# Optimization experiments

Hardware: AMD Instinct MI355X
Metric: run time of the kernel (lower is better)

Reference implementation:

```python
import jax, jax.numpy as jnp
import numpy as np

H, C = 3, 64  # heads, per-head channels
NEG_SLOPE = 0.2

def setup_inputs() -> dict:
    key = jax.random.key(0)
    ks = jax.random.split(key, 8)
    B, N, D, E = 2, 50000, 128, 800000
    h = jax.random.normal(ks[0], (B, N, D), dtype=jnp.float32)
    edge_index = jax.random.randint(ks[1], (2, E), 0, N, dtype=jnp.int64)
    s = 1.0 / np.sqrt(D)
    W = jax.random.normal(ks[2], (D, H * C), dtype=jnp.float32) * s
    a_src = jax.random.normal(ks[3], (H, C), dtype=jnp.float32) * (1.0 / np.sqrt(C))
    a_dst = jax.random.normal(ks[4], (H, C), dtype=jnp.float32) * (1.0 / np.sqrt(C))
    bias = jnp.zeros((H * C,), dtype=jnp.float32)
    Wo = jax.random.normal(ks[5], (H * C, 1), dtype=jnp.float32) * (1.0 / np.sqrt(H * C))
    bo = jnp.zeros((1,), dtype=jnp.float32)
    return {"h": h, "edge_index": edge_index, "W": W, "a_src": a_src,
            "a_dst": a_dst, "bias": bias, "Wo": Wo, "bo": bo}

def _gat_single(h_b, src, dst, N, W, a_src, a_dst, bias):
    # h_b: [N, D] -> x: [N, H, C]
    x = (h_b @ W).reshape(-1, H, C)
    alpha_s = jnp.einsum('nhc,hc->nh', x, a_src)  # [N, H]
    alpha_d = jnp.einsum('nhc,hc->nh', x, a_dst)  # [N, H]
    e = alpha_s[src] + alpha_d[dst]               # [E', H]
    e = jnp.where(e > 0, e, NEG_SLOPE * e)        # leaky_relu(0.2)
    # segment softmax over edges grouped by destination node
    emax = jax.ops.segment_max(e, dst, num_segments=N)          # [N, H]
    p = jnp.exp(e - emax[dst])
    denom = jax.ops.segment_sum(p, dst, num_segments=N)         # [N, H]
    att = p / (denom[dst] + 1e-16)                               # [E', H]
    out = jax.ops.segment_sum(att[:, :, None] * x[src], dst, num_segments=N)  # [N,H,C]
    return out.reshape(-1, H * C) + bias

def reference(h, edge_index, W, a_src, a_dst, bias, Wo, bo):
    B, N, D = h.shape
    # PyG GATConv default: add self loops
    loops = jnp.arange(N, dtype=edge_index.dtype)
    src = jnp.concatenate([edge_index[0], loops])
    dst = jnp.concatenate([edge_index[1], loops])
    gat = jax.vmap(lambda hb: _gat_single(hb, src, dst, N, W, a_src, a_dst, bias))(h)
    gat = jax.nn.elu(gat)            # [B, N, H*C]; dropout inactive (eval)
    logits = gat @ Wo + bo           # [B, N, 1]
    return logits
```

## Files before the change

### kernel.cpp

```cpp
#include <hip/hip_runtime.h>
#include <hip/hip_bf16.h>
#include <math.h>

typedef __hip_bfloat16 bf16;
typedef __attribute__((ext_vector_type(8))) short short8;
typedef __attribute__((ext_vector_type(4))) short short4v;
typedef __attribute__((ext_vector_type(4))) float f32x4;

#define HC 192
#define DIN 128
#define NEG_SLOPE 0.2f
#define GN 4
#define CAP 56
#define GROWS 128

static inline int cdiv(int a, int b){ return (a + b - 1) / b; }

__device__ inline short f2bf(float f){
  __hip_bfloat16 b = __float2bfloat16(f);
  return __builtin_bit_cast(short, b);
}
__device__ inline float loadf(const void* p, size_t i, int fm){
  return fm ? __bfloat162float(((const bf16*)p)[i]) : ((const float*)p)[i];
}
__device__ inline int eload(const void* p, long long i, int em){
  return em ? (int)(((const long long*)p)[i]) : ((const int*)p)[i];
}
__device__ inline unsigned pack2h(float a, float b){
  unsigned short ha = __builtin_bit_cast(unsigned short, (_Float16)a);
  unsigned short hb = __builtin_bit_cast(unsigned short, (_Float16)b);
  return (unsigned)ha | ((unsigned)hb << 16);
}
__device__ inline float unph(unsigned w, int hi){
  unsigned short hs = hi ? (unsigned short)(w >> 16) : (unsigned short)(w & 0xffff);
  return (float)__builtin_bit_cast(_Float16, hs);
}

__device__ inline int detect_fm(const unsigned* __restrict__ hw){
  unsigned w = hw[threadIdx.x & 63];
  unsigned expo = (w >> 7) & 0xFF;
  unsigned long long m = __ballot(expo >= 100 && expo <= 135);
  return __popcll(m) > 32;
}
__device__ inline int detect_em(const unsigned* __restrict__ ew){
  unsigned long long m = __ballot(ew[2*(threadIdx.x & 63) + 1] != 0);
  return __popcll(m) < 32;
}

__global__ void k_repack(const void* __restrict__ W, const void* __restrict__ a_src,
    const void* __restrict__ a_dst, const void* __restrict__ bias,
    const void* __restrict__ Wo, const void* __restrict__ bo,
    const unsigned* __restrict__ hw, bf16* __restrict__ Wt,
    float* __restrict__ asf, float* __restrict__ adf, float* __restrict__ biasf,
    float* __restrict__ Wof, float* __restrict__ bof,
    int* __restrict__ counts, int N){
  int fm = detect_fm(hw);
  int idx = blockIdx.x * 256 + threadIdx.x;
  for (int i = idx; i < N; i += 96 * 256) counts[i] = 0;
  if (idx < DIN * HC){
    int d = idx / HC, j = idx - d * HC;
    Wt[j * DIN + d] = __float2bfloat16(loadf(W, idx, fm));
  }
  if (idx < HC){
    asf[idx]   = loadf(a_src, idx, fm);
    adf[idx]   = loadf(a_dst, idx, fm);
    biasf[idx] = loadf(bias, idx, fm);
    Wof[idx]   = loadf(Wo, idx, fm);
  }
  if (idx == 0) bof[0] = loadf(bo, 0, fm);
}

__global__ __launch_bounds__(512) void k_gemm(const void* __restrict__ h,
    const bf16* __restrict__ Wt, bf16* __restrict__ x,
    const float* __restrict__ asf, const float* __restrict__ adf,
    float* __restrict__ asp, float* __restrict__ adp, int M, int N){
  int fm   = detect_fm((const unsigned*)h);
  int tid  = threadIdx.x;
  int w    = tid >> 6;
  int lane = tid & 63;
  int r16  = lane & 15;
  int quad = lane >> 4;
  __shared__ short ldsW[HC * 136];
  for (int c = tid; c < HC * 16; c += 512){
    int row = c >> 4, kg = c & 15;
    *(short8*)&ldsW[row * 136 + kg * 8] = *(const short8*)(Wt + row * DIN + kg * 8);
  }
  __syncthreads();

  int row  = blockIdx.x * GROWS + w * 16 + r16;
  int lrow = min(row, M - 1);
  f32x4 acc[12];
  #pragma unroll
  for (int i = 0; i < 12; i++) acc[i] = (f32x4){0.f,0.f,0.f,0.f};
  size_t hbase = (size_t)lrow * DIN + quad * 8;
  #pragma unroll
  for (int kb = 0; kb < 4; kb++){
    short8 bh;
    if (fm == 0){
      const float* hf = (const float*)h + hbase + kb * 32;
      float4 a = *(const float4*)hf;
      float4 b = *(const float4*)(hf + 4);
      bh[0]=f2bf(a.x); bh[1]=f2bf(a.y); bh[2]=f2bf(a.z); bh[3]=f2bf(a.w);
      bh[4]=f2bf(b.x); bh[5]=f2bf(b.y); bh[6]=f2bf(b.z); bh[7]=f2bf(b.w);
    } else {
      bh = *(const short8*)((const bf16*)h + hbase + kb * 32);
    }
    #pragma unroll
    for (int nt = 0; nt < 12; nt++){
      short8 aw = *(const short8*)&ldsW[(nt*16 + r16) * 136 + kb * 32 + quad * 8];
      acc[nt] = __builtin_amdgcn_mfma_f32_16x16x32_bf16(aw, bh, acc[nt], 0,0,0);
    }
  }
  if (row < M){
    #pragma unroll
    for (int nt = 0; nt < 12; nt++){
      short4v pk = { f2bf(acc[nt][0]), f2bf(acc[nt][1]),
                     f2bf(acc[nt][2]), f2bf(acc[nt][3]) };
      *(short4v*)(x + (size_t)row * HC + nt*16 + quad*4) = pk;
    }
  }
  float vs[3] = {0.f,0.f,0.f}, vd[3] = {0.f,0.f,0.f};
  #pragma unroll
  for (int nt = 0; nt < 12; nt++){
    int hh = nt >> 2;
    f32x4 a4 = *(const f32x4*)(asf + nt*16 + quad*4);
    f32x4 d4 = *(const f32x4*)(adf + nt*16 + quad*4);
    vs[hh] += acc[nt][0]*a4[0] + acc[nt][1]*a4[1] + acc[nt][2]*a4[2] + acc[nt][3]*a4[3];
    vd[hh] += acc[nt][0]*d4[0] + acc[nt][1]*d4[1] + acc[nt][2]*d4[2] + acc[nt][3]*d4[3];
  }
  #pragma unroll
  for (int hh = 0; hh < 3; hh++){
    float v1 = vs[hh], v2 = vd[hh];
    v1 += __shfl_down(v1, 32);  v1 += __shfl_down(v1, 16);
    v2 += __shfl_down(v2, 32);  v2 += __shfl_down(v2, 16);
    if (lane < 16 && row < M){
      int b = row >= N;
      int node = row - b * N;
      asp[(size_t)node*8 + b*3 + hh] = v1;
      adp[(size_t)node*8 + b*3 + hh] = v2;
    }
  }
}

__global__ void k_scatter(const void* __restrict__ ei, int E, int N,
    int* __restrict__ counts, const float* __restrict__ asp,
    const float* __restrict__ adp, uint4* __restrict__ pe){
  int em = detect_em((const unsigned*)ei);
  int idx = blockIdx.x * 256 + threadIdx.x;
  if (idx >= E + N) return;
  int s, d;
  if (idx < E){
    s = eload(ei, idx, em);
    d = eload(ei, (long long)E + idx, em);
  } else { s = d = idx - E; }
  if ((unsigned)d >= (unsigned)N) return;
  if ((unsigned)s >= (unsigned)N) s = 0;
  int slot = atomicAdd(&counts[d], 1);
  if (slot >= CAP) return;
  float4 A0 = ((const float4*)asp)[(size_t)s*2];
  float4 A1 = ((const float4*)asp)[(size_t)s*2 + 1];
  float4 D0 = ((const float4*)adp)[(size_t)d*2];
  float4 D1 = ((const float4*)adp)[(size_t)d*2 + 1];
  float e0 = A0.x + D0.x, e1 = A0.y + D0.y, e2 = A0.z + D0.z;
  float e3 = A0.w + D0.w, e4 = A1.x + D1.x, e5 = A1.y + D1.y;
  e0 = e0 > 0.f ? e0 : NEG_SLOPE*e0;  e1 = e1 > 0.f ? e1 : NEG_SLOPE*e1;
  e2 = e2 > 0.f ? e2 : NEG_SLOPE*e2;  e3 = e3 > 0.f ? e3 : NEG_SLOPE*e3;
  e4 = e4 > 0.f ? e4 : NEG_SLOPE*e4;  e5 = e5 > 0.f ? e5 : NEG_SLOPE*e5;
  uint4 rec;
  rec.x = pack2h(__expf(e0), __expf(e1));
  rec.y = pack2h(__expf(e2), __expf(e3));
  rec.z = pack2h(__expf(e4), __expf(e5));
  rec.w = (unsigned)s;
  pe[(size_t)d*CAP + slot] = rec;
}

__global__ __launch_bounds__(192) void k_gat(const bf16* __restrict__ x,
    const uint4* __restrict__ pe, const int* __restrict__ cnt,
    const float* __restrict__ biasf, const float* __restrict__ Wof,
    const float* __restrict__ bof, float* __restrict__ out, int N){
  int blk  = blockIdx.x;
  int t    = threadIdx.x;
  int node = t / 48;
  int u    = t - node * 48;
  int b    = u >= 24;
  int c8   = u - b * 24;
  int hh   = c8 >> 3;
  __shared__ int   cs[GN];
  __shared__ uint4 ldsR[GN * CAP];
  __shared__ float red[192];
  if (t < GN) cs[t] = min(cnt[GN*blk + t], CAP);
  __syncthreads();
  for (int j = t; j < GN * CAP; j += 192){
    int nd = j / CAP, sl = j - nd * CAP;
    if (sl < cs[nd]) ldsR[j] = pe[(size_t)(GN*blk + nd) * CAP + sl];
  }
  __syncthreads();
  int mycnt = cs[node];
  const ushort* xb = (const ushort*)x + (size_t)b * N * HC + c8 * 8;
  int pidx = b*3 + hh;
  int pw_i = pidx >> 1, pw_h = pidx & 1;
  const unsigned* ldsU = (const unsigned*)ldsR;
  float acc[8];
  #pragma unroll
  for (int k = 0; k < 8; k++) acc[k] = 0.f;
  float den = 0.f;
  int rbase = node * CAP;
  #pragma unroll 8
  for (int i = 0; i < mycnt; i++){
    int rec = rbase + i;
    float p = unph(ldsU[rec*4 + pw_i], pw_h);
    int s   = (int)ldsU[rec*4 + 3];
    uint4 q = *(const uint4*)(xb + (size_t)s * HC);
    den += p;
    acc[0] = fmaf(p, __uint_as_float(q.x << 16),         acc[0]);
    acc[1] = fmaf(p, __uint_as_float(q.x & 0xffff0000u), acc[1]);
    acc[2] = fmaf(p, __uint_as_float(q.y << 16),         acc[2]);
    acc[3] = fmaf(p, __uint_as_float(q.y & 0xffff0000u), acc[3]);
    acc[4] = fmaf(p, __uint_as_float(q.z << 16),         acc[4]);
    acc[5] = fmaf(p, __uint_as_float(q.z & 0xffff0000u), acc[5]);
    acc[6] = fmaf(p, __uint_as_float(q.w << 16),         acc[6]);
    acc[7] = fmaf(p, __uint_as_float(q.w & 0xffff0000u), acc[7]);
  }
  float inv = 1.f / (den + 1e-16f);
  float4 bi0 = ((const float4*)biasf)[c8*2], bi1 = ((const float4*)biasf)[c8*2+1];
  float4 w0  = ((const float4*)Wof)[c8*2],  w1  = ((const float4*)Wof)[c8*2+1];
  float r = 0.f;
  {
    float v;
    v = acc[0]*inv + bi0.x; v = v > 0.f ? v : expm1f(v); r += v * w0.x;
    v = acc[1]*inv + bi0.y; v = v > 0.f ? v : expm1f(v); r += v * w0.y;
    v = acc[2]*inv + bi0.z; v = v > 0.f ? v : expm1f(v); r += v * w0.z;
    v = acc[3]*inv + bi0.w; v = v > 0.f ? v : expm1f(v); r += v * w0.w;
    v = acc[4]*inv + bi1.x; v = v > 0.f ? v : expm1f(v); r += v * w1.x;
    v = acc[5]*inv + bi1.y; v = v > 0.f ? v : expm1f(v); r += v * w1.y;
    v = acc[6]*inv + bi1.z; v = v > 0.f ? v : expm1f(v); r += v * w1.z;
    v = acc[7]*inv + bi1.w; v = v > 0.f ? v : expm1f(v); r += v * w1.w;
  }
  red[t] = r;
  __syncthreads();
  if (t < 64){
    int g = t >> 3, l = t & 7;
    float v = red[g*24 + l] + red[g*24 + 8 + l] + red[g*24 + 16 + l];
    v += __shfl_down(v, 4, 8);
    v += __shfl_down(v, 2, 8);
    v += __shfl_down(v, 1, 8);
    if (l == 0){
      int nd = GN*blk + (g >> 1);
      int bb = g & 1;
      out[(size_t)bb * N + nd] = v + bof[0];
    }
  }
}

extern "C" void kernel_launch(void* const* d_in, const int* in_sizes, int n_in,
                              void* d_out, int out_size, void* d_ws, size_t ws_size,
                              hipStream_t stream){
  const void* h     = d_in[0];
  const void* ei    = d_in[1];
  const void* W     = d_in[2];
  const void* a_src = d_in[3];
  const void* a_dst = d_in[4];
  const void* bias  = d_in[5];
  const void* Wo    = d_in[6];
  const void* bo    = d_in[7];
  float* out = (float*)d_out;

  const int M    = in_sizes[0] / DIN;
  const int N    = M / 2;
  const int E    = in_sizes[1] / 2;
  const int Etot = E + N;

  char* ws = (char*)d_ws;
  size_t off = 0;
  auto alloc = [&](size_t bytes) -> void* {
    void* p = ws + off;
    off = (off + bytes + 511) & ~(size_t)511;
    return p;
  };
  bf16*  x       = (bf16*) alloc((size_t)M * HC * sizeof(bf16));
  float* asp     = (float*)alloc((size_t)N * 8 * sizeof(float));
  float* adp     = (float*)alloc((size_t)N * 8 * sizeof(float));
  int*   counts  = (int*)  alloc((size_t)N * sizeof(int));
  uint4* pe      = (uint4*)alloc((size_t)N * CAP * sizeof(uint4));
  bf16*  Wt      = (bf16*) alloc((size_t)DIN * HC * sizeof(bf16));
  float* asf     = (float*)alloc(HC * sizeof(float));
  float* adf     = (float*)alloc(HC * sizeof(float));
  float* biasf   = (float*)alloc(HC * sizeof(float));
  float* Wof     = (float*)alloc(HC * sizeof(float));
  float* bof     = (float*)alloc(16 * sizeof(float));
  (void)ws_size; (void)n_in; (void)out_size;

  k_repack<<<96, 256, 0, stream>>>(W, a_src, a_dst, bias, Wo, bo,
      (const unsigned*)h, Wt, asf, adf, biasf, Wof, bof, counts, N);
  k_gemm<<<cdiv(M, GROWS), 512, 0, stream>>>(h, Wt, x, asf, adf, asp, adp, M, N);
  k_scatter<<<cdiv(Etot, 256), 256, 0, stream>>>(ei, E, N, counts, asp, adp, pe);
  k_gat<<<N / GN, 192, 0, stream>>>(x, pe, counts, biasf, Wof, bof, out, N);
}
```

Before: 264.2 us.

## Bucket edge sources only and recompute attention logits inside aggregation kernel

```diff
diff --git a/kernel.cpp b/kernel.cpp
--- a/kernel.cpp
+++ b/kernel.cpp
@@ -25,15 +25,6 @@
 }
 __device__ inline int eload(const void* p, long long i, int em){
   return em ? (int)(((const long long*)p)[i]) : ((const int*)p)[i];
-}
-__device__ inline unsigned pack2h(float a, float b){
-  unsigned short ha = __builtin_bit_cast(unsigned short, (_Float16)a);
-  unsigned short hb = __builtin_bit_cast(unsigned short, (_Float16)b);
-  return (unsigned)ha | ((unsigned)hb << 16);
-}
-__device__ inline float unph(unsigned w, int hi){
-  unsigned short hs = hi ? (unsigned short)(w >> 16) : (unsigned short)(w & 0xffff);
-  return (float)__builtin_bit_cast(_Float16, hs);
 }
 
 __device__ inline int detect_fm(const unsigned* __restrict__ hw){
@@ -68,6 +59,23 @@
     Wof[idx]   = loadf(Wo, idx, fm);
   }
   if (idx == 0) bof[0] = loadf(bo, 0, fm);
+}
+
+__global__ void k_bucket(const void* __restrict__ ei, int E, int N,
+    int* __restrict__ counts, unsigned* __restrict__ srcs){
+  int em = detect_em((const unsigned*)ei);
+  int idx = blockIdx.x * 256 + threadIdx.x;
+  if (idx >= E + N) return;
+  int s, d;
+  if (idx < E){
+    s = eload(ei, idx, em);
+    d = eload(ei, (long long)E + idx, em);
+  } else { s = d = idx - E; }
+  if ((unsigned)d >= (unsigned)N) return;
+  if ((unsigned)s >= (unsigned)N) s = 0;
+  int slot = atomicAdd(&counts[d], 1);
+  if (slot >= CAP) return;
+  srcs[(size_t)d * CAP + slot] = (unsigned)s;
 }
 
 __global__ __launch_bounds__(512) void k_gemm(const void* __restrict__ h,
@@ -112,11 +120,14 @@
     }
   }
   if (row < M){
+    int bb    = row >= N;
+    int nodeR = row - bb * N;
+    bf16* xr  = x + ((size_t)nodeR * 2 + bb) * HC;
     #pragma unroll
     for (int nt = 0; nt < 12; nt++){
       short4v pk = { f2bf(acc[nt][0]), f2bf(acc[nt][1]),
                      f2bf(acc[nt][2]), f2bf(acc[nt][3]) };
-      *(short4v*)(x + (size_t)row * HC + nt*16 + quad*4) = pk;
+      *(short4v*)(xr + nt*16 + quad*4) = pk;
     }
   }
   float vs[3] = {0.f,0.f,0.f}, vd[3] = {0.f,0.f,0.f};
@@ -142,40 +153,9 @@
   }
 }
 
-__global__ void k_scatter(const void* __restrict__ ei, int E, int N,
-    int* __restrict__ counts, const float* __restrict__ asp,
-    const float* __restrict__ adp, uint4* __restrict__ pe){
-  int em = detect_em((const unsigned*)ei);
-  int idx = blockIdx.x * 256 + threadIdx.x;
-  if (idx >= E + N) return;
-  int s, d;
-  if (idx < E){
-    s = eload(ei, idx, em);
-    d = eload(ei, (long long)E + idx, em);
-  } else { s = d = idx - E; }
-  if ((unsigned)d >= (unsigned)N) return;
-  if ((unsigned)s >= (unsigned)N) s = 0;
-  int slot = atomicAdd(&counts[d], 1);
-  if (slot >= CAP) return;
-  float4 A0 = ((const float4*)asp)[(size_t)s*2];
-  float4 A1 = ((const float4*)asp)[(size_t)s*2 + 1];
-  float4 D0 = ((const float4*)adp)[(size_t)d*2];
-  float4 D1 = ((const float4*)adp)[(size_t)d*2 + 1];
-  float e0 = A0.x + D0.x, e1 = A0.y + D0.y, e2 = A0.z + D0.z;
-  float e3 = A0.w + D0.w, e4 = A1.x + D1.x, e5 = A1.y + D1.y;
-  e0 = e0 > 0.f ? e0 : NEG_SLOPE*e0;  e1 = e1 > 0.f ? e1 : NEG_SLOPE*e1;
-  e2 = e2 > 0.f ? e2 : NEG_SLOPE*e2;  e3 = e3 > 0.f ? e3 : NEG_SLOPE*e3;
-  e4 = e4 > 0.f ? e4 : NEG_SLOPE*e4;  e5 = e5 > 0.f ? e5 : NEG_SLOPE*e5;
-  uint4 rec;
-  rec.x = pack2h(__expf(e0), __expf(e1));
-  rec.y = pack2h(__expf(e2), __expf(e3));
-  rec.z = pack2h(__expf(e4), __expf(e5));
-  rec.w = (unsigned)s;
-  pe[(size_t)d*CAP + slot] = rec;
-}
-
 __global__ __launch_bounds__(192) void k_gat(const bf16* __restrict__ x,
-    const uint4* __restrict__ pe, const int* __restrict__ cnt,
+    const unsigned* __restrict__ srcs, const int* __restrict__ cnt,
+    const float* __restrict__ asp, const float* __restrict__ adp,
     const float* __restrict__ biasf, const float* __restrict__ Wof,
     const float* __restrict__ bof, float* __restrict__ out, int N){
   int blk  = blockIdx.x;
@@ -185,21 +165,21 @@
   int b    = u >= 24;
   int c8   = u - b * 24;
   int hh   = c8 >> 3;
-  __shared__ int   cs[GN];
-  __shared__ uint4 ldsR[GN * CAP];
-  __shared__ float red[192];
+  __shared__ int      cs[GN];
+  __shared__ unsigned ldsS[GN * CAP];
+  __shared__ float    red[192];
   if (t < GN) cs[t] = min(cnt[GN*blk + t], CAP);
   __syncthreads();
   for (int j = t; j < GN * CAP; j += 192){
     int nd = j / CAP, sl = j - nd * CAP;
-    if (sl < cs[nd]) ldsR[j] = pe[(size_t)(GN*blk + nd) * CAP + sl];
+    if (sl < cs[nd]) ldsS[j] = srcs[(size_t)(GN*blk + nd) * CAP + sl];
   }
   __syncthreads();
   int mycnt = cs[node];
-  const ushort* xb = (const ushort*)x + (size_t)b * N * HC + c8 * 8;
-  int pidx = b*3 + hh;
-  int pw_i = pidx >> 1, pw_h = pidx & 1;
-  const unsigned* ldsU = (const unsigned*)ldsR;
+  int d     = GN*blk + node;
+  int pidx  = b*3 + hh;
+  float adv = adp[(size_t)d * 8 + pidx];
+  const ushort* xb = (const ushort*)x + (size_t)b * HC + c8 * 8;
   float acc[8];
   #pragma unroll
   for (int k = 0; k < 8; k++) acc[k] = 0.f;
@@ -207,10 +187,11 @@
   int rbase = node * CAP;
   #pragma unroll 8
   for (int i = 0; i < mycnt; i++){
-    int rec = rbase + i;
-    float p = unph(ldsU[rec*4 + pw_i], pw_h);
-    int s   = (int)ldsU[rec*4 + 3];
-    uint4 q = *(const uint4*)(xb + (size_t)s * HC);
+    int s   = (int)ldsS[rbase + i];
+    float e = asp[(size_t)s * 8 + pidx] + adv;
+    e = e > 0.f ? e : NEG_SLOPE * e;
+    float p = __expf(e);
+    uint4 q = *(const uint4*)(xb + (size_t)s * (2 * HC));
     den += p;
     acc[0] = fmaf(p, __uint_as_float(q.x << 16),         acc[0]);
     acc[1] = fmaf(p, __uint_as_float(q.x & 0xffff0000u), acc[1]);
@@ -277,22 +258,22 @@
     off = (off + bytes + 511) & ~(size_t)511;
     return p;
   };
-  bf16*  x       = (bf16*) alloc((size_t)M * HC * sizeof(bf16));
-  float* asp     = (float*)alloc((size_t)N * 8 * sizeof(float));
-  float* adp     = (float*)alloc((size_t)N * 8 * sizeof(float));
-  int*   counts  = (int*)  alloc((size_t)N * sizeof(int));
-  uint4* pe      = (uint4*)alloc((size_t)N * CAP * sizeof(uint4));
-  bf16*  Wt      = (bf16*) alloc((size_t)DIN * HC * sizeof(bf16));
-  float* asf     = (float*)alloc(HC * sizeof(float));
-  float* adf     = (float*)alloc(HC * sizeof(float));
-  float* biasf   = (float*)alloc(HC * sizeof(float));
-  float* Wof     = (float*)alloc(HC * sizeof(float));
-  float* bof     = (float*)alloc(16 * sizeof(float));
+  bf16*     x      = (bf16*)    alloc((size_t)M * HC * sizeof(bf16));
+  float*    asp    = (float*)   alloc((size_t)N * 8 * sizeof(float));
+  float*    adp    = (float*)   alloc((size_t)N * 8 * sizeof(float));
+  int*      counts = (int*)     alloc((size_t)N * sizeof(int));
+  unsigned* srcs   = (unsigned*)alloc((size_t)N * CAP * sizeof(unsigned));
+  bf16*     Wt     = (bf16*)    alloc((size_t)DIN * HC * sizeof(bf16));
+  float*    asf    = (float*)   alloc(HC * sizeof(float));
+  float*    adf    = (float*)   alloc(HC * sizeof(float));
+  float*    biasf  = (float*)   alloc(HC * sizeof(float));
+  float*    Wof    = (float*)   alloc(HC * sizeof(float));
+  float*    bof    = (float*)   alloc(16 * sizeof(float));
   (void)ws_size; (void)n_in; (void)out_size;
 
   k_repack<<<96, 256, 0, stream>>>(W, a_src, a_dst, bias, Wo, bo,
       (const unsigned*)h, Wt, asf, adf, biasf, Wof, bof, counts, N);
+  k_bucket<<<cdiv(Etot, 256), 256, 0, stream>>>(ei, E, N, counts, srcs);
   k_gemm<<<cdiv(M, GROWS), 512, 0, stream>>>(h, Wt, x, asf, adf, asp, adp, M, N);
-  k_scatter<<<cdiv(Etot, 256), 256, 0, stream>>>(ei, E, N, counts, asp, adp, pe);
-  k_gat<<<N / GN, 192, 0, stream>>>(x, pe, counts, biasf, Wof, bof, out, N);
-}
+  k_gat<<<N / GN, 192, 0, stream>>>(x, srcs, counts, asp, adp, biasf, Wof, bof, out, N);
+}
```

After: 280.9 us. +6.3%, slower.

## Precompute attention logits via folded W·a, overlap edge bucketing with GEMM

Applied to the files above, without the earlier changes.

```diff
diff --git a/kernel.cpp b/kernel.cpp
--- a/kernel.cpp
+++ b/kernel.cpp
@@ -47,47 +47,152 @@
   return __popcll(m) < 32;
 }
 
-__global__ void k_repack(const void* __restrict__ W, const void* __restrict__ a_src,
+__global__ void k_zero(const void* __restrict__ W, const void* __restrict__ a_src,
     const void* __restrict__ a_dst, const void* __restrict__ bias,
     const void* __restrict__ Wo, const void* __restrict__ bo,
-    const unsigned* __restrict__ hw, bf16* __restrict__ Wt,
-    float* __restrict__ asf, float* __restrict__ adf, float* __restrict__ biasf,
-    float* __restrict__ Wof, float* __restrict__ bof,
-    int* __restrict__ counts, int N){
-  int fm = detect_fm(hw);
-  int idx = blockIdx.x * 256 + threadIdx.x;
-  for (int i = idx; i < N; i += 96 * 256) counts[i] = 0;
-  if (idx < DIN * HC){
-    int d = idx / HC, j = idx - d * HC;
-    Wt[j * DIN + d] = __float2bfloat16(loadf(W, idx, fm));
-  }
-  if (idx < HC){
-    asf[idx]   = loadf(a_src, idx, fm);
-    adf[idx]   = loadf(a_dst, idx, fm);
-    biasf[idx] = loadf(bias, idx, fm);
-    Wof[idx]   = loadf(Wo, idx, fm);
-  }
-  if (idx == 0) bof[0] = loadf(bo, 0, fm);
-}
-
-__global__ __launch_bounds__(512) void k_gemm(const void* __restrict__ h,
-    const bf16* __restrict__ Wt, bf16* __restrict__ x,
-    const float* __restrict__ asf, const float* __restrict__ adf,
-    float* __restrict__ asp, float* __restrict__ adp, int M, int N){
+    const unsigned* __restrict__ hw, int* __restrict__ counts,
+    float* __restrict__ biasf, float* __restrict__ Wof, float* __restrict__ bof,
+    float* __restrict__ wasg, float* __restrict__ wadg, int N){
+  int fm  = detect_fm(hw);
+  int bid = blockIdx.x, t = threadIdx.x;
+  if (bid == 0){
+    if (t < HC){ biasf[t] = loadf(bias, t, fm); Wof[t] = loadf(Wo, t, fm); }
+    if (t == 255) bof[0] = loadf(bo, 0, fm);
+    return;
+  }
+  if (bid == 1 || bid == 2){
+    const void* av = (bid == 1) ? a_src : a_dst;
+    float* dst     = (bid == 1) ? wasg  : wadg;
+    for (int j = t; j < 384; j += 256){
+      int d = j & 127, hh = j >> 7;
+      float acc = 0.f;
+      #pragma unroll 8
+      for (int c = 0; c < 64; c++)
+        acc += loadf(W, (size_t)d * HC + hh * 64 + c, fm) * loadf(av, hh * 64 + c, fm);
+      dst[hh * 128 + d] = acc;
+    }
+    return;
+  }
+  for (int i = (bid - 3) * 256 + t; i < N; i += 37 * 256) counts[i] = 0;
+}
+
+__global__ __launch_bounds__(256) void k_pre(const void* __restrict__ h,
+    const void* __restrict__ ei, const float* __restrict__ wasg,
+    const float* __restrict__ wadg, float* __restrict__ asp,
+    float* __restrict__ adp, int* __restrict__ counts,
+    unsigned* __restrict__ srcs, int M, int N, int E, int AB){
+  int bid = blockIdx.x, t = threadIdx.x;
+  if (bid >= AB){
+    int em  = detect_em((const unsigned*)ei);
+    int idx = (bid - AB) * 256 + t;
+    if (idx >= E + N) return;
+    int s, d;
+    if (idx < E){
+      s = eload(ei, idx, em);
+      d = eload(ei, (long long)E + idx, em);
+    } else { s = d = idx - E; }
+    if ((unsigned)d >= (unsigned)N) return;
+    if ((unsigned)s >= (unsigned)N) s = 0;
+    int slot = atomicAdd(&counts[d], 1);
+    if (slot >= CAP) return;
+    srcs[(size_t)d * CAP + slot] = (unsigned)s;
+    return;
+  }
+  int fm = detect_fm((const unsigned*)h);
+  __shared__ float wl[768];
+  for (int j = t; j < 768; j += 256)
+    wl[j] = (j < 384) ? wasg[j] : wadg[j - 384];
+  __syncthreads();
+  int r   = t >> 3;
+  int i   = t & 7;
+  int row = bid * 32 + r;
+  if (row >= M) return;
+  int c0  = i * 16;
+  float hv[16];
+  if (fm == 0){
+    const float4* hp = (const float4*)((const float*)h + (size_t)row * DIN + c0);
+    float4 v0 = hp[0], v1 = hp[1], v2 = hp[2], v3 = hp[3];
+    hv[0]=v0.x; hv[1]=v0.y; hv[2]=v0.z; hv[3]=v0.w;
+    hv[4]=v1.x; hv[5]=v1.y; hv[6]=v1.z; hv[7]=v1.w;
+    hv[8]=v2.x; hv[9]=v2.y; hv[10]=v2.z; hv[11]=v2.w;
+    hv[12]=v3.x; hv[13]=v3.y; hv[14]=v3.z; hv[15]=v3.w;
+  } else {
+    const short8* sp = (const short8*)((const bf16*)h + (size_t)row * DIN + c0);
+    short8 s0 = sp[0], s1 = sp[1];
+    #pragma unroll
+    for (int k = 0; k < 8; k++){
+      hv[k]   = __bfloat162float(__builtin_bit_cast(bf16, s0[k]));
+      hv[k+8] = __bfloat162float(__builtin_bit_cast(bf16, s1[k]));
+    }
+  }
+  float vs0=0.f, vs1=0.f, vs2=0.f, vd0=0.f, vd1=0.f, vd2=0.f;
+  #pragma unroll
+  for (int k = 0; k < 16; k++){
+    float hvk = hv[k];
+    int d = c0 + k;
+    vs0 += hvk * wl[d];        vs1 += hvk * wl[128 + d];  vs2 += hvk * wl[256 + d];
+    vd0 += hvk * wl[384 + d];  vd1 += hvk * wl[512 + d];  vd2 += hvk * wl[640 + d];
+  }
+  #pragma unroll
+  for (int m = 1; m < 8; m <<= 1){
+    vs0 += __shfl_xor(vs0, m);  vs1 += __shfl_xor(vs1, m);  vs2 += __shfl_xor(vs2, m);
+    vd0 += __shfl_xor(vd0, m);  vd1 += __shfl_xor(vd1, m);  vd2 += __shfl_xor(vd2, m);
+  }
+  if (i == 0){
+    int b    = row >= N;
+    int node = row - b * N;
+    float* ap = asp + (size_t)node * 8 + b * 3;
+    float* dp = adp + (size_t)node * 8 + b * 3;
+    ap[0] = vs0; ap[1] = vs1; ap[2] = vs2;
+    dp[0] = vd0; dp[1] = vd1; dp[2] = vd2;
+  }
+}
+
+__global__ __launch_bounds__(512) void k_fused(const void* __restrict__ h,
+    const void* __restrict__ W, bf16* __restrict__ x,
+    const float* __restrict__ asp, const float* __restrict__ adp,
+    const int* __restrict__ counts, const unsigned* __restrict__ srcs,
+    uint4* __restrict__ pe, int M, int N, int NBG){
+  __shared__ alignas(16) short ldsW[HC * 136];
+  int bid = blockIdx.x, tid = threadIdx.x;
+  if (bid >= NBG){
+    int j = (bid - NBG) * 512 + tid;
+    if (j >= N * CAP) return;
+    int nd = j / CAP, sl = j - nd * CAP;
+    if (sl >= min(counts[nd], CAP)) return;
+    int s = (int)srcs[j];
+    float4 A0 = ((const float4*)asp)[(size_t)s*2];
+    float4 A1 = ((const float4*)asp)[(size_t)s*2 + 1];
+    float4 D0 = ((const float4*)adp)[(size_t)nd*2];
+    float4 D1 = ((const float4*)adp)[(size_t)nd*2 + 1];
+    float e0 = A0.x + D0.x, e1 = A0.y + D0.y, e2 = A0.z + D0.z;
+    float e3 = A0.w + D0.w, e4 = A1.x + D1.x, e5 = A1.y + D1.y;
+    e0 = e0 > 0.f ? e0 : NEG_SLOPE*e0;  e1 = e1 > 0.f ? e1 : NEG_SLOPE*e1;
+    e2 = e2 > 0.f ? e2 : NEG_SLOPE*e2;  e3 = e3 > 0.f ? e3 : NEG_SLOPE*e3;
+    e4 = e4 > 0.f ? e4 : NEG_SLOPE*e4;  e5 = e5 > 0.f ? e5 : NEG_SLOPE*e5;
+    uint4 rec;
+    rec.x = pack2h(__expf(e0), __expf(e1));
+    rec.y = pack2h(__expf(e2), __expf(e3));
+    rec.z = pack2h(__expf(e4), __expf(e5));
+    rec.w = (unsigned)s;
+    pe[j] = rec;
+    return;
+  }
   int fm   = detect_fm((const unsigned*)h);
-  int tid  = threadIdx.x;
   int w    = tid >> 6;
   int lane = tid & 63;
   int r16  = lane & 15;
   int quad = lane >> 4;
-  __shared__ short ldsW[HC * 136];
-  for (int c = tid; c < HC * 16; c += 512){
-    int row = c >> 4, kg = c & 15;
-    *(short8*)&ldsW[row * 136 + kg * 8] = *(const short8*)(Wt + row * DIN + kg * 8);
-  }
-  __syncthreads();
-
-  int row  = blockIdx.x * GROWS + w * 16 + r16;
+  for (int pi = tid; pi < HC * 16; pi += 512){
+    int j = pi % HC, dblk = pi / HC;
+    short8 v8;
+    #pragma unroll
+    for (int kk = 0; kk < 8; kk++)
+      v8[kk] = f2bf(loadf(W, (size_t)(dblk*8 + kk) * HC + j, fm));
+    *(short8*)&ldsW[j * 136 + dblk * 8] = v8;
+  }
+  __syncthreads();
+  int row  = bid * GROWS + w * 16 + r16;
   int lrow = min(row, M - 1);
   f32x4 acc[12];
   #pragma unroll
@@ -112,66 +217,14 @@
     }
   }
   if (row < M){
+    bf16* xr = x + (size_t)row * HC;
     #pragma unroll
     for (int nt = 0; nt < 12; nt++){
       short4v pk = { f2bf(acc[nt][0]), f2bf(acc[nt][1]),
                      f2bf(acc[nt][2]), f2bf(acc[nt][3]) };
-      *(short4v*)(x + (size_t)row * HC + nt*16 + quad*4) = pk;
-    }
-  }
-  float vs[3] = {0.f,0.f,0.f}, vd[3] = {0.f,0.f,0.f};
-  #pragma unroll
-  for (int nt = 0; nt < 12; nt++){
-    int hh = nt >> 2;
-    f32x4 a4 = *(const f32x4*)(asf + nt*16 + quad*4);
-    f32x4 d4 = *(const f32x4*)(adf + nt*16 + quad*4);
-    vs[hh] += acc[nt][0]*a4[0] + acc[nt][1]*a4[1] + acc[nt][2]*a4[2] + acc[nt][3]*a4[3];
-    vd[hh] += acc[nt][0]*d4[0] + acc[nt][1]*d4[1] + acc[nt][2]*d4[2] + acc[nt][3]*d4[3];
-  }
-  #pragma unroll
-  for (int hh = 0; hh < 3; hh++){
-    float v1 = vs[hh], v2 = vd[hh];
-    v1 += __shfl_down(v1, 32);  v1 += __shfl_down(v1, 16);
-    v2 += __shfl_down(v2, 32);  v2 += __shfl_down(v2, 16);
-    if (lane < 16 && row < M){
-      int b = row >= N;
-      int node = row - b * N;
-      asp[(size_t)node*8 + b*3 + hh] = v1;
-      adp[(size_t)node*8 + b*3 + hh] = v2;
-    }
-  }
-}
-
-__global__ void k_scatter(const void* __restrict__ ei, int E, int N,
-    int* __restrict__ counts, const float* __restrict__ asp,
-    const float* __restrict__ adp, uint4* __restrict__ pe){
-  int em = detect_em((const unsigned*)ei);
-  int idx = blockIdx.x * 256 + threadIdx.x;
-  if (idx >= E + N) return;
-  int s, d;
-  if (idx < E){
-    s = eload(ei, idx, em);
-    d = eload(ei, (long long)E + idx, em);
-  } else { s = d = idx - E; }
-  if ((unsigned)d >= (unsigned)N) return;
-  if ((unsigned)s >= (unsigned)N) s = 0;
-  int slot = atomicAdd(&counts[d], 1);
-  if (slot >= CAP) return;
-  float4 A0 = ((const float4*)asp)[(size_t)s*2];
-  float4 A1 = ((const float4*)asp)[(size_t)s*2 + 1];
-  float4 D0 = ((const float4*)adp)[(size_t)d*2];
-  float4 D1 = ((const float4*)adp)[(size_t)d*2 + 1];
-  float e0 = A0.x + D0.x, e1 = A0.y + D0.y, e2 = A0.z + D0.z;
-  float e3 = A0.w + D0.w, e4 = A1.x + D1.x, e5 = A1.y + D1.y;
-  e0 = e0 > 0.f ? e0 : NEG_SLOPE*e0;  e1 = e1 > 0.f ? e1 : NEG_SLOPE*e1;
-  e2 = e2 > 0.f ? e2 : NEG_SLOPE*e2;  e3 = e3 > 0.f ? e3 : NEG_SLOPE*e3;
-  e4 = e4 > 0.f ? e4 : NEG_SLOPE*e4;  e5 = e5 > 0.f ? e5 : NEG_SLOPE*e5;
-  uint4 rec;
-  rec.x = pack2h(__expf(e0), __expf(e1));
-  rec.y = pack2h(__expf(e2), __expf(e3));
-  rec.z = pack2h(__expf(e4), __expf(e5));
-  rec.w = (unsigned)s;
-  pe[(size_t)d*CAP + slot] = rec;
+      *(short4v*)(xr + nt*16 + quad*4) = pk;
+    }
+  }
 }
 
 __global__ __launch_bounds__(192) void k_gat(const bf16* __restrict__ x,
@@ -277,22 +330,29 @@
     off = (off + bytes + 511) & ~(size_t)511;
     return p;
   };
-  bf16*  x       = (bf16*) alloc((size_t)M * HC * sizeof(bf16));
-  float* asp     = (float*)alloc((size_t)N * 8 * sizeof(float));
-  float* adp     = (float*)alloc((size_t)N * 8 * sizeof(float));
-  int*   counts  = (int*)  alloc((size_t)N * sizeof(int));
-  uint4* pe      = (uint4*)alloc((size_t)N * CAP * sizeof(uint4));
-  bf16*  Wt      = (bf16*) alloc((size_t)DIN * HC * sizeof(bf16));
-  float* asf     = (float*)alloc(HC * sizeof(float));
-  float* adf     = (float*)alloc(HC * sizeof(float));
-  float* biasf   = (float*)alloc(HC * sizeof(float));
-  float* Wof     = (float*)alloc(HC * sizeof(float));
-  float* bof     = (float*)alloc(16 * sizeof(float));
+  bf16*     x      = (bf16*)    alloc((size_t)M * HC * sizeof(bf16));
+  float*    asp    = (float*)   alloc((size_t)N * 8 * sizeof(float));
+  float*    adp    = (float*)   alloc((size_t)N * 8 * sizeof(float));
+  int*      counts = (int*)     alloc((size_t)N * sizeof(int));
+  unsigned* srcs   = (unsigned*)alloc((size_t)N * CAP * sizeof(unsigned));
+  uint4*    pe     = (uint4*)   alloc((size_t)N * CAP * sizeof(uint4));
+  float*    biasf  = (float*)   alloc(HC * sizeof(float));
+  float*    Wof    = (float*)   alloc(HC * sizeof(float));
+  float*    bof    = (float*)   alloc(16 * sizeof(float));
+  float*    wasg   = (float*)   alloc(384 * sizeof(float));
+  float*    wadg   = (float*)   alloc(384 * sizeof(float));
   (void)ws_size; (void)n_in; (void)out_size;
 
-  k_repack<<<96, 256, 0, stream>>>(W, a_src, a_dst, bias, Wo, bo,
-      (const unsigned*)h, Wt, asf, adf, biasf, Wof, bof, counts, N);
-  k_gemm<<<cdiv(M, GROWS), 512, 0, stream>>>(h, Wt, x, asf, adf, asp, adp, M, N);
-  k_scatter<<<cdiv(Etot, 256), 256, 0, stream>>>(ei, E, N, counts, asp, adp, pe);
+  const int AB  = cdiv(M, 32);
+  const int BB  = cdiv(Etot, 256);
+  const int NBG = cdiv(M, GROWS);
+  const int SC  = cdiv(N * CAP, 512);
+
+  k_zero<<<40, 256, 0, stream>>>(W, a_src, a_dst, bias, Wo, bo,
+      (const unsigned*)h, counts, biasf, Wof, bof, wasg, wadg, N);
+  k_pre<<<AB + BB, 256, 0, stream>>>(h, ei, wasg, wadg, asp, adp,
+      counts, srcs, M, N, E, AB);
+  k_fused<<<NBG + SC, 512, 0, stream>>>(h, W, x, asp, adp,
+      counts, srcs, pe, M, N, NBG);
   k_gat<<<N / GN, 192, 0, stream>>>(x, pe, counts, biasf, Wof, bof, out, N);
 }
```

Measured after the change: 322.3 us. 1.22x slower.
